# Kernel optimization log

Hardware: AMD Instinct MI355X
Metric: run time of the kernel (lower is better)

Reference implementation:

```python
import jax, jax.numpy as jnp
import numpy as np

B, S, D, H = 2, 4096, 256, 4
DH = D // H  # 64


def setup_inputs() -> dict:
    key = jax.random.key(0)
    ks = jax.random.split(key, 7)
    scale = 1.0 / np.sqrt(DH)  # torch Linear default init range ~ U(-1/sqrt(in), 1/sqrt(in))
    def w(k):
        return jax.random.uniform(k, (H, DH, DH), jnp.float32, -scale, scale)
    def b(k):
        return jax.random.uniform(k, (H, DH), jnp.float32, -scale, scale)
    return {
        "sequences": jax.random.normal(ks[0], (B, S, D), jnp.float32),
        "qw": w(ks[1]), "qb": b(ks[2]),
        "kw": w(ks[3]), "kb": b(ks[4]),
        "vw": w(ks[5]), "vb": b(ks[6]),
        "train": 0,
    }


def reference(sequences, qw, qb, kw, kb, vw, vb, train):
    # sequences: [B, S, D] -> per-head slices [B, H, S, DH]
    x = sequences.reshape(B, S, H, DH).transpose(0, 2, 1, 3)  # [B,H,S,DH]
    # torch Linear: y = x @ W.T + b, W: [out, in]
    q = jnp.einsum('bhsd,hed->bhse', x, qw) + qb[None, :, None, :]
    k = jnp.einsum('bhsd,hed->bhse', x, kw) + kb[None, :, None, :]
    v = jnp.einsum('bhsd,hed->bhse', x, vw) + vb[None, :, None, :]
    scores = jnp.einsum('bhqd,bhkd->bhqk', q, k) / jnp.sqrt(jnp.float32(DH))
    attn = jax.nn.softmax(scores, axis=-1)  # [B,H,S,S]
    out = jnp.einsum('bhqk,bhkd->bhqd', attn, v)  # [B,H,S,DH]
    # hstack over heads == concatenate head outputs along feature dim
    return out.transpose(0, 2, 1, 3).reshape(B, S, D)
```

## Files before the change

### kernel.cpp

```cpp
#include <hip/hip_runtime.h>
#include <hip/hip_bf16.h>
#include <hip/hip_fp16.h>


#define B_   2
#define S_   4096
#define D_   256
#define H_   4
#define DH_  64
#define BH_  8
#define NTOK (BH_*S_*DH_)

#define KVB  64
#define QW   32
#define NW   8
#define QB   (QW*NW)
#define NINST (BH_*(S_/QW))

typedef short v8s __attribute__((ext_vector_type(8)));
typedef float v16f __attribute__((ext_vector_type(16)));
typedef float v4f __attribute__((ext_vector_type(4)));
typedef unsigned v4u __attribute__((ext_vector_type(4)));
typedef unsigned v2u __attribute__((ext_vector_type(2)));
typedef int v2i __attribute__((ext_vector_type(2)));

#define QSCL (0.125f * 1.4426950408889634f)

static __device__ __forceinline__ short f2bf(float f) {
    __hip_bfloat16 h = __float2bfloat16(f);
    return *reinterpret_cast<short*>(&h);
}
static __device__ __forceinline__ unsigned cvtpk(float lo, float hi) {
    unsigned r;
    asm("v_cvt_pk_bf16_f32 %0, %1, %2" : "=v"(r) : "v"(lo), "v"(hi));
    return r;
}
static __device__ __forceinline__ float fexp2(float x) {
#if __has_builtin(__builtin_amdgcn_exp2f)
    return __builtin_amdgcn_exp2f(x);
#else
    float r;
    asm("v_exp_f32 %0, %1" : "=v"(r) : "v"(x));
    return r;
#endif
}
static __device__ __forceinline__ void pl32swap(unsigned &a, unsigned &b) {
#if __has_builtin(__builtin_amdgcn_permlane32_swap)
    v2i r = __builtin_amdgcn_permlane32_swap((int)a, (int)b, false, false);
    a = (unsigned)r[0]; b = (unsigned)r[1];
#else
    asm volatile("v_permlane32_swap_b32 %0, %1" : "+v"(a), "+v"(b));
#endif
}
static __device__ __forceinline__ float xadd32(float x) {
    unsigned a = __builtin_bit_cast(unsigned, x), b = a;
    pl32swap(a, b);
    return __builtin_bit_cast(float, a) + __builtin_bit_cast(float, b);
}
static __device__ __forceinline__ v16f vz16() {
    v16f z;
    #pragma unroll
    for (int i = 0; i < 16; ++i) z[i] = 0.f;
    return z;
}
static __device__ __forceinline__ v8s cvt8(const float* p) {
    v4f f0 = *(const v4f*)(p);
    v4f f1 = *(const v4f*)(p + 4);
    v4u u = { cvtpk(f0[0], f0[1]), cvtpk(f0[2], f0[3]),
              cvtpk(f1[0], f1[1]), cvtpk(f1[2], f1[3]) };
    return __builtin_bit_cast(v8s, u);
}

__global__ __launch_bounds__(128) void qkv_proj_mfma(
    const float* __restrict__ x,
    const float* __restrict__ qw, const float* __restrict__ qb,
    const float* __restrict__ kw, const float* __restrict__ kb,
    const float* __restrict__ vw, const float* __restrict__ vb,
    short* __restrict__ Qo, short* __restrict__ Ko, short* __restrict__ Vt)
{
    const int t   = threadIdx.x;
    const int w   = t >> 6;
    const int l   = t & 63;
    const int l31 = l & 31, lhi = l >> 5;
    const int bh  = blockIdx.y, h = bh & 3, b = bh >> 2;
    const int s0  = blockIdx.x * 32;

    const float* xrow = x + ((size_t)(b*S_ + s0 + l31))*D_ + h*DH_;
    v8s af[4];
    #pragma unroll
    for (int k0 = 0; k0 < 4; ++k0)
        af[k0] = cvt8(xrow + k0*16 + lhi*8);

    const float* Wp[3] = { qw + h*DH_*DH_, kw + h*DH_*DH_, vw + h*DH_*DH_ };
    const float* Bp[3] = { qb + h*DH_,     kb + h*DH_,     vb + h*DH_ };
    short* Qh = Qo + (size_t)bh*S_*DH_;
    short* Kh = Ko + (size_t)bh*S_*DH_;

    #pragma unroll
    for (int ui = 0; ui < 3; ++ui) {
        const int u  = w*3 + ui;
        const int p  = u >> 1;
        const int eb = u & 1;
        const int e  = eb*32 + l31;
        const float* wrow = Wp[p] + e*DH_;

        v16f acc = vz16();
        #pragma unroll
        for (int k0 = 0; k0 < 4; ++k0) {
            v8s bfr = cvt8(wrow + k0*16 + lhi*8);
            acc = __builtin_amdgcn_mfma_f32_32x32x16_bf16(af[k0], bfr, acc, 0, 0, 0);
        }

        const float bias = Bp[p][e];
        if (p == 0) {
            const float bq = bias * QSCL;
            #pragma unroll
            for (int r = 0; r < 16; ++r) acc[r] = fmaf(acc[r], QSCL, bq);
        } else {
            #pragma unroll
            for (int r = 0; r < 16; ++r) acc[r] += bias;
        }

        if (p < 2) {
            short* dst = (p == 0) ? Qh : Kh;
            #pragma unroll
            for (int r = 0; r < 16; ++r) {
                int s = s0 + (r & 3) + 8*(r >> 2) + 4*lhi;
                dst[(size_t)s*DH_ + e] = f2bf(acc[r]);
            }
        } else {
            short* vtb = Vt + (size_t)bh*DH_*S_ + (size_t)e*S_;
            #pragma unroll
            for (int rq = 0; rq < 4; ++rq) {
                v2u pr = { cvtpk(acc[rq*4+0], acc[rq*4+1]),
                           cvtpk(acc[rq*4+2], acc[rq*4+3]) };
                int s = s0 + rq*8 + 4*lhi;
                *(v2u*)(vtb + s) = pr;
            }
        }
    }
}

__global__ __launch_bounds__(512, 4) void attn_kernel(
    const short* __restrict__ Q, const short* __restrict__ K,
    const short* __restrict__ Vt, _Float16* __restrict__ Opart,
    float* __restrict__ Ml, int nspl, int kvlen)
{
    __shared__ __align__(16) short klds[2][64][64];
    __shared__ __align__(16) short vlds[2][64][64];

    const int t    = threadIdx.x;
    const int w    = t >> 6;
    const int l    = t & 63;
    const int l31  = l & 31;
    const int lhi  = l >> 5;
    const int bh   = blockIdx.y;
    const int qtil = blockIdx.x;
    const int spl  = blockIdx.z;
    const int q0   = qtil*QB + w*QW;
    const int kv_beg = spl * kvlen;

    const short* Qh = Q  + (size_t)bh*S_*DH_;
    const short* Kh = K  + (size_t)bh*S_*DH_;
    const short* Vh = Vt + (size_t)bh*DH_*S_;

    const int rl  = l >> 3;
    const int cs  = (l & 7) ^ (rl & 7);
    const size_t koff = (size_t)(w*8 + rl)*DH_ + cs*8;
    const size_t voff = (size_t)(w*8 + rl)*S_  + cs*8;
    const int ldst = w*512 + l*8;

    v8s qf[4];
    #pragma unroll
    for (int k0 = 0; k0 < 4; ++k0)
        qf[k0] = *(const v8s*)(Qh + (size_t)(q0 + l31)*DH_ + k0*16 + lhi*8);

    int fo[2][4];
    #pragma unroll
    for (int a = 0; a < 2; ++a)
        #pragma unroll
        for (int c = 0; c < 4; ++c)
            fo[a][c] = (a*32 + l31)*64 + (((c*2 + lhi) ^ (l31 & 7))*8);

    v16f o0 = vz16(), o1 = vz16();
    float l_run = 0.f;

    const int NT = kvlen / KVB;

    {
        v8s k0v = *(const v8s*)(Kh + (size_t)kv_beg*DH_ + koff);
        v8s v0v = *(const v8s*)(Vh + kv_beg + voff);
        *(v8s*)((short*)klds[0] + ldst) = k0v;
        *(v8s*)((short*)vlds[0] + ldst) = v0v;
    }
    __syncthreads();

    for (int it = 0; it < NT; ++it) {
        const int cur = it & 1;

        v8s knx, vnx;
        if (it + 1 < NT) {
            size_t kvn = kv_beg + (size_t)(it+1)*KVB;
            knx = *(const v8s*)(Kh + kvn*DH_ + koff);
            vnx = *(const v8s*)(Vh + kvn + voff);
        }

        const short* kb = (const short*)klds[cur];
        const short* vb = (const short*)vlds[cur];

        v16f s0 = vz16(), s1 = vz16();
        __builtin_amdgcn_s_setprio(1);
        #pragma unroll
        for (int k0 = 0; k0 < 4; ++k0) {
            v8s a0 = *(const v8s*)(kb + fo[0][k0]);
            v8s a1 = *(const v8s*)(kb + fo[1][k0]);
            s0 = __builtin_amdgcn_mfma_f32_32x32x16_bf16(a0, qf[k0], s0, 0, 0, 0);
            s1 = __builtin_amdgcn_mfma_f32_32x32x16_bf16(a1, qf[k0], s1, 0, 0, 0);
        }
        __builtin_amdgcn_s_setprio(0);

        #pragma unroll
        for (int i = 0; i < 16; ++i) s0[i] = fexp2(s0[i]);
        #pragma unroll
        for (int i = 0; i < 16; ++i) s1[i] = fexp2(s1[i]);
        float a16[16];
        #pragma unroll
        for (int i = 0; i < 16; ++i) a16[i] = s0[i] + s1[i];
        #pragma unroll
        for (int st = 8; st; st >>= 1)
            #pragma unroll
            for (int i = 0; i < st; ++i) a16[i] += a16[i+st];
        l_run += xadd32(a16[0]);

        unsigned pwv[4][4];
        {
            unsigned j0 = cvtpk(s0[0], s0[1]),  j1 = cvtpk(s0[2], s0[3]);
            unsigned j2 = cvtpk(s0[4], s0[5]),  j3 = cvtpk(s0[6], s0[7]);
            unsigned j4 = cvtpk(s0[8], s0[9]),  j5 = cvtpk(s0[10], s0[11]);
            unsigned j6 = cvtpk(s0[12], s0[13]), j7 = cvtpk(s0[14], s0[15]);
            pl32swap(j0, j2); pl32swap(j1, j3);
            pwv[0][0] = j0; pwv[0][1] = j1; pwv[0][2] = j2; pwv[0][3] = j3;
            pl32swap(j4, j6); pl32swap(j5, j7);
            pwv[1][0] = j4; pwv[1][1] = j5; pwv[1][2] = j6; pwv[1][3] = j7;
        }
        {
            unsigned j0 = cvtpk(s1[0], s1[1]),  j1 = cvtpk(s1[2], s1[3]);
            unsigned j2 = cvtpk(s1[4], s1[5]),  j3 = cvtpk(s1[6], s1[7]);
            unsigned j4 = cvtpk(s1[8], s1[9]),  j5 = cvtpk(s1[10], s1[11]);
            unsigned j6 = cvtpk(s1[12], s1[13]), j7 = cvtpk(s1[14], s1[15]);
            pl32swap(j0, j2); pl32swap(j1, j3);
            pwv[2][0] = j0; pwv[2][1] = j1; pwv[2][2] = j2; pwv[2][3] = j3;
            pl32swap(j4, j6); pl32swap(j5, j7);
            pwv[3][0] = j4; pwv[3][1] = j5; pwv[3][2] = j6; pwv[3][3] = j7;
        }

        __builtin_amdgcn_s_setprio(1);
        #pragma unroll
        for (int kk = 0; kk < 4; ++kk) {
            v4u u = { pwv[kk][0], pwv[kk][1], pwv[kk][2], pwv[kk][3] };
            v8s pf = __builtin_bit_cast(v8s, u);
            v8s va0 = *(const v8s*)(vb + fo[0][kk]);
            v8s va1 = *(const v8s*)(vb + fo[1][kk]);
            o0 = __builtin_amdgcn_mfma_f32_32x32x16_bf16(va0, pf, o0, 0, 0, 0);
            o1 = __builtin_amdgcn_mfma_f32_32x32x16_bf16(va1, pf, o1, 0, 0, 0);
        }
        __builtin_amdgcn_s_setprio(0);

        if (it + 1 < NT) {
            *(v8s*)((short*)klds[cur^1] + ldst) = knx;
            *(v8s*)((short*)vlds[cur^1] + ldst) = vnx;
        }
        __syncthreads();
    }

    const int inst = bh*(S_/QW) + qtil*NW + w;
    _Float16* od = Opart + ((size_t)inst*nspl + spl)*2048;
    #pragma unroll
    for (int r = 0; r < 16; ++r) od[r*64 + l]      = (_Float16)o0[r];
    #pragma unroll
    for (int r = 0; r < 16; ++r) od[(16+r)*64 + l] = (_Float16)o1[r];
    Ml[((size_t)inst*nspl + spl)*64 + l] = (l < 32) ? 0.f : l_run;
}

template<int NSPL>
__global__ __launch_bounds__(256) void combine_kernel(
    const _Float16* __restrict__ Opart, const float* __restrict__ Ml,
    float* __restrict__ out)
{
    const int t = threadIdx.x;
    const int w = t >> 6, l = t & 63;
    const int inst = blockIdx.x*4 + w;
    const int bh = inst >> 7;
    const int qw = inst & 127;
    const int b = bh >> 2, h = bh & 3;
    const int l31 = l & 31, lhi = l >> 5;
    const int q = qw*32 + l31;

    const float* mlp = Ml + (size_t)inst*NSPL*64;
    float L = 0.f;
    #pragma unroll
    for (int sp = 0; sp < NSPL; ++sp)
        L += mlp[sp*64 + 32 + l31];
    float inv = 1.f / L;

    const _Float16* op0 = Opart + (size_t)inst*NSPL*2048;
    float* outp = out + ((size_t)(b*S_ + q))*D_ + h*DH_;

    #pragma unroll
    for (int g = 0; g < 8; ++g) {
        v4f acc;
        #pragma unroll
        for (int jj = 0; jj < 4; ++jj) {
            int r = g*4 + jj;
            float v = 0.f;
            #pragma unroll
            for (int sp = 0; sp < NSPL; ++sp)
                v += (float)op0[sp*2048 + r*64 + l];
            acc[jj] = v * inv;
        }
        int td = g >> 2, gg = g & 3;
        int d = td*32 + gg*8 + lhi*4;
        *(v4f*)(outp + d) = acc;
    }
}

extern "C" void kernel_launch(void* const* d_in, const int* in_sizes, int n_in,
                              void* d_out, int out_size, void* d_ws, size_t ws_size,
                              hipStream_t stream)
{
    const float* x  = (const float*)d_in[0];
    const float* qw = (const float*)d_in[1];
    const float* qb = (const float*)d_in[2];
    const float* kw = (const float*)d_in[3];
    const float* kb = (const float*)d_in[4];
    const float* vw = (const float*)d_in[5];
    const float* vb = (const float*)d_in[6];

    short* Qb  = (short*)d_ws;
    short* Kb  = Qb + NTOK;
    short* Vtb = Kb + NTOK;
    _Float16* Opart = (_Float16*)(Vtb + NTOK);

    size_t base = (size_t)3*NTOK*sizeof(short);
    size_t per_spl = (size_t)NINST*2048*2 + (size_t)NINST*64*4;
    int nspl = 1;
    if      (ws_size >= base + 4*per_spl) nspl = 4;
    else if (ws_size >= base + 2*per_spl) nspl = 2;
    float* Ml = (float*)(Opart + (size_t)NINST*nspl*2048);
    int kvlen = S_/nspl;

    float* out = (float*)d_out;

    dim3 pg(S_/32, BH_), pb(128);
    hipLaunchKernelGGL(qkv_proj_mfma, pg, pb, 0, stream,
                       x, qw, qb, kw, kb, vw, vb, Qb, Kb, Vtb);

    dim3 ag(S_/QB, BH_, nspl), ab(512);
    hipLaunchKernelGGL(attn_kernel, ag, ab, 0, stream, Qb, Kb, Vtb, Opart, Ml, nspl, kvlen);

    dim3 cg(NINST/4), cb(256);
    if (nspl == 4)
        hipLaunchKernelGGL(combine_kernel<4>, cg, cb, 0, stream, Opart, Ml, out);
    else if (nspl == 2)
        hipLaunchKernelGGL(combine_kernel<2>, cg, cb, 0, stream, Opart, Ml, out);
    else
        hipLaunchKernelGGL(combine_kernel<1>, cg, cb, 0, stream, Opart, Ml, out);
}
```

Measured before the change: 62.20 us.

## Fuse split-KV combine into attention kernel via per-instance atomic counters

Removes the separate combine kernel launch. Each attention wave writes its partial output and row sum, issues a fence and bumps a per-query-tile atomic counter. The last split to arrive sums the partials and writes the normalized output. This saves one launch and its dependency gap, at the cost of an extra memset, atomics and fences, and a combine tail that runs on the last-arriving wave with a runtime-length split loop.

```diff
diff --git a/kernel.cpp b/kernel.cpp
--- a/kernel.cpp
+++ b/kernel.cpp
@@ -144,7 +144,8 @@
 __global__ __launch_bounds__(512, 4) void attn_kernel(
     const short* __restrict__ Q, const short* __restrict__ K,
     const short* __restrict__ Vt, _Float16* __restrict__ Opart,
-    float* __restrict__ Ml, int nspl, int kvlen)
+    float* __restrict__ Ml, int* __restrict__ ctr,
+    float* __restrict__ out, int nspl, int kvlen)
 {
     __shared__ __align__(16) short klds[2][64][64];
     __shared__ __align__(16) short vlds[2][64][64];
@@ -274,53 +275,49 @@
     }
 
     const int inst = bh*(S_/QW) + qtil*NW + w;
-    _Float16* od = Opart + ((size_t)inst*nspl + spl)*2048;
-    #pragma unroll
-    for (int r = 0; r < 16; ++r) od[r*64 + l]      = (_Float16)o0[r];
-    #pragma unroll
-    for (int r = 0; r < 16; ++r) od[(16+r)*64 + l] = (_Float16)o1[r];
-    Ml[((size_t)inst*nspl + spl)*64 + l] = (l < 32) ? 0.f : l_run;
-}
-
-template<int NSPL>
-__global__ __launch_bounds__(256) void combine_kernel(
-    const _Float16* __restrict__ Opart, const float* __restrict__ Ml,
-    float* __restrict__ out)
-{
-    const int t = threadIdx.x;
-    const int w = t >> 6, l = t & 63;
-    const int inst = blockIdx.x*4 + w;
-    const int bh = inst >> 7;
-    const int qw = inst & 127;
-    const int b = bh >> 2, h = bh & 3;
-    const int l31 = l & 31, lhi = l >> 5;
-    const int q = qw*32 + l31;
-
-    const float* mlp = Ml + (size_t)inst*NSPL*64;
-    float L = 0.f;
-    #pragma unroll
-    for (int sp = 0; sp < NSPL; ++sp)
-        L += mlp[sp*64 + 32 + l31];
-    float inv = 1.f / L;
-
-    const _Float16* op0 = Opart + (size_t)inst*NSPL*2048;
-    float* outp = out + ((size_t)(b*S_ + q))*D_ + h*DH_;
-
-    #pragma unroll
-    for (int g = 0; g < 8; ++g) {
-        v4f acc;
-        #pragma unroll
-        for (int jj = 0; jj < 4; ++jj) {
-            int r = g*4 + jj;
-            float v = 0.f;
-            #pragma unroll
-            for (int sp = 0; sp < NSPL; ++sp)
-                v += (float)op0[sp*2048 + r*64 + l];
-            acc[jj] = v * inv;
-        }
-        int td = g >> 2, gg = g & 3;
-        int d = td*32 + gg*8 + lhi*4;
-        *(v4f*)(outp + d) = acc;
+    {
+        _Float16* od = Opart + ((size_t)inst*nspl + spl)*2048;
+        #pragma unroll
+        for (int r = 0; r < 16; ++r) od[r*64 + l]      = (_Float16)o0[r];
+        #pragma unroll
+        for (int r = 0; r < 16; ++r) od[(16+r)*64 + l] = (_Float16)o1[r];
+        Ml[((size_t)inst*nspl + spl)*64 + l] = (l < 32) ? 0.f : l_run;
+    }
+
+    __threadfence();
+    int old = 0;
+    if (l == 0) old = atomicAdd(&ctr[inst], 1);
+    old = __shfl(old, 0);
+
+    if (old == nspl - 1) {
+        __threadfence();
+
+        const float* mlp = Ml + (size_t)inst*nspl*64;
+        float L = 0.f;
+        for (int sp = 0; sp < nspl; ++sp)
+            L += mlp[sp*64 + 32 + l31];
+        float inv = 1.f / L;
+
+        const _Float16* op0 = Opart + (size_t)inst*nspl*2048;
+        const int bh_ = inst >> 7;
+        const int qw_ = inst & 127;
+        float* outp = out + ((size_t)((bh_ >> 2)*S_ + qw_*32 + l31))*D_
+                          + (bh_ & 3)*DH_;
+
+        #pragma unroll
+        for (int g = 0; g < 8; ++g) {
+            v4f acc;
+            #pragma unroll
+            for (int jj = 0; jj < 4; ++jj) {
+                int r = g*4 + jj;
+                float v = 0.f;
+                for (int sp = 0; sp < nspl; ++sp)
+                    v += (float)op0[sp*2048 + r*64 + l];
+                acc[jj] = v * inv;
+            }
+            int d = (g >> 2)*32 + (g & 3)*8 + lhi*4;
+            *(v4f*)(outp + d) = acc;
+        }
     }
 }
 
@@ -343,26 +340,23 @@
 
     size_t base = (size_t)3*NTOK*sizeof(short);
     size_t per_spl = (size_t)NINST*2048*2 + (size_t)NINST*64*4;
+    size_t ctr_bytes = (size_t)NINST*4;
     int nspl = 1;
-    if      (ws_size >= base + 4*per_spl) nspl = 4;
-    else if (ws_size >= base + 2*per_spl) nspl = 2;
+    if      (ws_size >= base + 4*per_spl + ctr_bytes) nspl = 4;
+    else if (ws_size >= base + 2*per_spl + ctr_bytes) nspl = 2;
     float* Ml = (float*)(Opart + (size_t)NINST*nspl*2048);
+    int* ctr = (int*)(Ml + (size_t)NINST*nspl*64);
     int kvlen = S_/nspl;
 
     float* out = (float*)d_out;
+
+    hipMemsetAsync(ctr, 0, ctr_bytes, stream);
 
     dim3 pg(S_/32, BH_), pb(128);
     hipLaunchKernelGGL(qkv_proj_mfma, pg, pb, 0, stream,
                        x, qw, qb, kw, kb, vw, vb, Qb, Kb, Vtb);
 
     dim3 ag(S_/QB, BH_, nspl), ab(512);
-    hipLaunchKernelGGL(attn_kernel, ag, ab, 0, stream, Qb, Kb, Vtb, Opart, Ml, nspl, kvlen);
-
-    dim3 cg(NINST/4), cb(256);
-    if (nspl == 4)
-        hipLaunchKernelGGL(combine_kernel<4>, cg, cb, 0, stream, Opart, Ml, out);
-    else if (nspl == 2)
-        hipLaunchKernelGGL(combine_kernel<2>, cg, cb, 0, stream, Opart, Ml, out);
-    else
-        hipLaunchKernelGGL(combine_kernel<1>, cg, cb, 0, stream, Opart, Ml, out);
-}
+    hipLaunchKernelGGL(attn_kernel, ag, ab, 0, stream, Qb, Kb, Vtb,
+                       Opart, Ml, ctr, out, nspl, kvlen);
+}
```

Measured after the change: 213.2 us. +242.8%, slower.
